# Kernel tuning notes

Measured on AMD Instinct MI355X. Metric: run time of the kernel, lower is better.

Reference implementation:

```python
import jax, jax.numpy as jnp
import numpy as np

NUM_EXPERTS = 8
TOP_K = 2
N_EMBD = 1024
BLOCKING = 128
D_FFN = ((4 * N_EMBD // TOP_K) + BLOCKING - 1) // BLOCKING * BLOCKING  # 2048


def setup_inputs() -> dict:
    key = jax.random.key(0)
    k_x, k_r, k_w1, k_w2 = jax.random.split(key, 4)
    B, S = 4, 2048
    x = jax.random.normal(k_x, (B, S, N_EMBD), dtype=jnp.float32)
    # nn.Linear weight layout: [out_features, in_features]
    router_w = jax.random.normal(k_r, (NUM_EXPERTS, N_EMBD), dtype=jnp.float32) * 0.02
    # trunc_normal(std=0.02, a=-0.06, b=0.06) approximated by clipped normal
    w1 = jnp.clip(jax.random.normal(k_w1, (N_EMBD, NUM_EXPERTS * D_FFN), dtype=jnp.float32) * 0.02, -0.06, 0.06)
    w2 = jnp.clip(jax.random.normal(k_w2, (NUM_EXPERTS * D_FFN, N_EMBD), dtype=jnp.float32) * 0.02, -0.06, 0.06)
    return {"x": x, "router_w": router_w, "w1": w1, "w2": w2}


def reference(x, router_w, w1, w2):
    B, S, D = x.shape
    T = B * S
    x_flat = x.reshape(T, D)

    # Router
    router_logits = x_flat @ router_w.T                       # [T, E]
    router_probs = jax.nn.softmax(router_logits.astype(jnp.float32), axis=-1)
    expert_weights, selected_experts = jax.lax.top_k(router_probs, TOP_K)  # [T, K]
    expert_weights = expert_weights / expert_weights.sum(axis=-1, keepdims=True)
    expert_weights = expert_weights.astype(x.dtype)

    # Combine weights c[t, e] = sum_k weight[t, k] * [sel[t, k] == e]
    combine = jnp.zeros((T, NUM_EXPERTS), dtype=x.dtype)
    combine = combine.at[jnp.arange(T)[:, None], selected_experts].add(expert_weights)

    # Expert FFNs (math equivalent of block-sparse sdd/gelu/dsd + scatter-combine)
    w1r = w1.reshape(D, NUM_EXPERTS, D_FFN)
    w2r = w2.reshape(NUM_EXPERTS, D_FFN, D)
    out_flat = jnp.zeros((T, D), dtype=x.dtype)
    for e in range(NUM_EXPERTS):
        h = jax.nn.gelu(x_flat @ w1r[:, e, :], approximate=False)  # [T, d_ffn]
        out_flat = out_flat + combine[:, e:e + 1] * (h @ w2r[e])
    output = out_flat.reshape(B, S, D)

    # Aux losses
    router_z_loss = jnp.mean(jax.nn.logsumexp(router_logits, axis=-1) ** 2)
    p_i = router_probs.mean(axis=0)                           # [E]
    f_i = jnp.zeros((NUM_EXPERTS,), dtype=x.dtype).at[selected_experts.reshape(-1)].add(
        jnp.float32(1.0) / (T * TOP_K))
    load_balance_loss = NUM_EXPERTS * jnp.dot(f_i, p_i.astype(x.dtype))

    return output, router_z_loss, load_balance_loss, f_i
```

## Files before the change

### kernel.cpp

```cpp
#include <hip/hip_runtime.h>
#include <hip/hip_bf16.h>
#include <math.h>

#define T_TOK   8192
#define D_MODEL 1024
#define DFFN    2048
#define N_EXP   8
#define NASSIGN (T_TOK*2)

#define TM 256
#define BN 256
#define BK 64
#define TILE_MAX 72

#define WS_ZSUM     0
#define WS_PSUM     4
#define WS_COUNTS   64
#define WS_CURSOR   96
#define WS_OFFS     128
#define WS_NTILES   160
#define WS_QHEAD    164
#define WS_QTOTAL   168
#define WS_DONE1    256
#define WS_TMAP     1024
#define WS_QITEMS   2560
#define WS_SEL      8192
#define WS_WGT      73728
#define WS_AIDX     139264
#define WS_AW       204800
#define WS_XB       270336
#define WS_W1T      (WS_XB + 16777216)
#define WS_W2T      (WS_W1T + 33554432)
#define WS_H        (WS_W2T + 33554432)

typedef __attribute__((ext_vector_type(8))) short bf16x8;
typedef __attribute__((ext_vector_type(4))) float f32x4;
typedef __attribute__((ext_vector_type(4))) unsigned int u32x4;

static __device__ __forceinline__ unsigned short f2bf(float f) {
    unsigned int u = __builtin_bit_cast(unsigned int, f);
    u += 0x7fffu + ((u >> 16) & 1u);
    return (unsigned short)(u >> 16);
}

static __device__ __forceinline__ void gll16(const unsigned short* g, unsigned short* l) {
    __builtin_amdgcn_global_load_lds(
        (const __attribute__((address_space(1))) unsigned int*)g,
        (__attribute__((address_space(3))) unsigned int*)l, 16, 0, 0);
}

static __device__ __forceinline__ int frag_off(int row, int kc) {
    return (row * 8 + (kc ^ (row & 7))) * 8;
}

__global__ __launch_bounds__(256) void transpose_cvt_kernel(
    const float* __restrict__ in, unsigned short* __restrict__ out, int K, int N)
{
    int e = blockIdx.z;
    const float* inp = in + (size_t)e * K * N;
    unsigned short* outp = out + (size_t)e * K * N;
    __shared__ unsigned short tile[64][68];
    int k0 = blockIdx.y * 64, n0 = blockIdx.x * 64;
    int tid = threadIdx.x;
    int r = tid >> 4, c4 = (tid & 15) * 4;
    #pragma unroll
    for (int p = 0; p < 4; ++p) {
        int k = r + p * 16;
        float4 v = *(const float4*)(inp + (size_t)(k0 + k) * N + n0 + c4);
        tile[k][c4+0] = f2bf(v.x);
        tile[k][c4+1] = f2bf(v.y);
        tile[k][c4+2] = f2bf(v.z);
        tile[k][c4+3] = f2bf(v.w);
    }
    __syncthreads();
    int n = tid >> 2, kc = (tid & 3) * 16;
    unsigned short t[16];
    #pragma unroll
    for (int j = 0; j < 16; ++j) t[j] = tile[kc + j][n];
    unsigned short* o = outp + (size_t)(n0 + n) * K + k0 + kc;
    *(u32x4*)o       = *(u32x4*)t;
    *(u32x4*)(o + 8) = *(u32x4*)(t + 8);
}

__global__ __launch_bounds__(256) void router_kernel(
    const float* __restrict__ x, const float* __restrict__ rw,
    float* zsum, float* psum, int* counts, int* sel, float* wgt,
    unsigned short* __restrict__ xb)
{
    __shared__ float xs[32*129];
    __shared__ float rs[8*129];
    __shared__ float lg[32*9];
    __shared__ float blk_p[8];
    __shared__ int   blk_c[8];
    __shared__ float blk_z;
    int tid = threadIdx.x;
    if (tid < 8) { blk_p[tid] = 0.f; blk_c[tid] = 0; }
    if (tid == 8) blk_z = 0.f;
    int tb = blockIdx.x * 32;
    int tt = tid >> 3, e = tid & 7;
    float acc = 0.f;
    for (int c = 0; c < 8; ++c) {
        int c0 = c * 128;
        #pragma unroll
        for (int p = 0; p < 16; ++p) {
            int flat = p * 256 + tid;
            int r = flat >> 7, col = flat & 127;
            xs[r*129 + col] = x[(size_t)(tb + r)*D_MODEL + c0 + col];
        }
        #pragma unroll
        for (int p = 0; p < 4; ++p) {
            int flat = p * 256 + tid;
            int er = flat >> 7, col = flat & 127;
            rs[er*129 + col] = rw[(size_t)er*D_MODEL + c0 + col];
        }
        __syncthreads();
        {
            int rr = tid >> 3, cc = (tid & 7) * 16;
            unsigned short tmp[16];
            #pragma unroll
            for (int j = 0; j < 16; ++j) tmp[j] = f2bf(xs[rr*129 + cc + j]);
            unsigned short* o = xb + (size_t)(tb + rr)*D_MODEL + c0 + cc;
            *(u32x4*)o       = *(u32x4*)tmp;
            *(u32x4*)(o + 8) = *(u32x4*)(tmp + 8);
        }
        #pragma unroll 8
        for (int i = 0; i < 128; ++i)
            acc += xs[tt*129 + i] * rs[e*129 + i];
        __syncthreads();
    }
    lg[tt*9 + e] = acc;
    __syncthreads();
    if (tid < 32) {
        int t = tb + tid;
        float l[8], p[8];
        float mx = -1e30f;
        #pragma unroll
        for (int j = 0; j < 8; ++j) { l[j] = lg[tid*9 + j]; mx = fmaxf(mx, l[j]); }
        float se = 0.f;
        #pragma unroll
        for (int j = 0; j < 8; ++j) { p[j] = expf(l[j] - mx); se += p[j]; }
        float inv = 1.f / se;
        #pragma unroll
        for (int j = 0; j < 8; ++j) p[j] *= inv;
        float lse = mx + logf(se);
        atomicAdd(&blk_z, lse*lse);
        #pragma unroll
        for (int j = 0; j < 8; ++j) atomicAdd(&blk_p[j], p[j]);
        int i0 = 0; float b0 = p[0];
        #pragma unroll
        for (int j = 1; j < 8; ++j) if (p[j] > b0) { b0 = p[j]; i0 = j; }
        int i1 = -1; float b1 = -1.f;
        #pragma unroll
        for (int j = 0; j < 8; ++j) if (j != i0 && p[j] > b1) { b1 = p[j]; i1 = j; }
        float s = b0 + b1;
        sel[t*2+0] = i0; sel[t*2+1] = i1;
        wgt[t*2+0] = b0 / s; wgt[t*2+1] = b1 / s;
        atomicAdd(&blk_c[i0], 1); atomicAdd(&blk_c[i1], 1);
    }
    __syncthreads();
    if (tid < 8) {
        atomicAdd(&counts[tid], blk_c[tid]);
        unsafeAtomicAdd(&psum[tid], blk_p[tid]);
    }
    if (tid == 8) unsafeAtomicAdd(zsum, blk_z);
}

__global__ void finalize_kernel(const int* counts, const float* psum, const float* zsum,
                                int* offs, int* ntiles, int* tmap, int* qitems,
                                int* qtotal, float* out_tail)
{
    if (threadIdx.x != 0) return;
    int off = 0, nt = 0;
    float lb = 0.f;
    for (int e = 0; e < N_EXP; ++e) {
        int c = counts[e];
        offs[e] = off;
        for (int m0 = 0; m0 < c; m0 += TM) {
            tmap[nt*4+0] = e;
            tmap[nt*4+1] = off + m0;
            tmap[nt*4+2] = min(TM, c - m0);
            tmap[nt*4+3] = 0;
            nt++;
        }
        float fi = (float)c / (float)NASSIGN;
        out_tail[2 + e] = fi;
        lb += fi * (psum[e] / (float)T_TOK);
        off += c;
    }
    *ntiles = nt;
    int q = 0;
    for (int t = 0; t < nt; ++t)
        for (int nb = 0; nb < DFFN/BN; ++nb)
            qitems[q++] = (0 << 14) | (t << 4) | nb;
    for (int t = 0; t < nt; ++t)
        for (int nb = 0; nb < D_MODEL/BN; ++nb)
            qitems[q++] = (1 << 14) | (t << 4) | nb;
    *qtotal = q;
    out_tail[0] = zsum[0] / (float)T_TOK;
    out_tail[1] = (float)N_EXP * lb;
}

__global__ __launch_bounds__(256) void scatter_kernel(
    const int* __restrict__ sel, const float* __restrict__ wgt,
    const int* __restrict__ offs, int* cursor, int* aidx, float* aw)
{
    int t = blockIdx.x * 256 + threadIdx.x;
    if (t >= T_TOK) return;
    #pragma unroll
    for (int k = 0; k < 2; ++k) {
        int e = sel[t*2 + k];
        int pos = atomicAdd(&cursor[e], 1);
        int r = offs[e] + pos;
        aidx[r] = t;
        aw[r] = wgt[t*2 + k];
    }
}


static __device__ __forceinline__ void gemm1_tile(
    int e, int gr, int valid, int n0,
    const unsigned short* __restrict__ xb, const unsigned short* __restrict__ w1t,
    const int* __restrict__ aidx, unsigned short* __restrict__ H,
    unsigned short (*As)[TM*BK], unsigned short (*Bs)[TM*BK], int tid)
{
    int lane = tid & 63, wave = tid >> 6;
    int wm = (wave >> 2) * 128, wn = (wave & 3) * 64;
    int q = lane >> 4, r16 = lane & 15;
    f32x4 acc[8][4];
    #pragma unroll
    for (int i = 0; i < 8; ++i)
        #pragma unroll
        for (int j = 0; j < 4; ++j) acc[i][j] = (f32x4){0.f, 0.f, 0.f, 0.f};

    const unsigned short* aga[4];
    const unsigned short* bga[4];
    int coff[4];
    #pragma unroll
    for (int u = 0; u < 4; ++u) {
        int cc = tid + u*512;
        int m = cc >> 3, kl = cc & 7;
        int kg = kl ^ (m & 7);
        int tok = aidx[gr + min(m, valid - 1)];
        aga[u] = xb + (size_t)tok * D_MODEL + kg*8;
        bga[u] = w1t + ((size_t)(e * DFFN + n0 + m)) * D_MODEL + kg*8;
        coff[u] = cc * 8;
    }

    const int NK = D_MODEL / BK;
    #pragma unroll
    for (int u = 0; u < 4; ++u) gll16(aga[u], &As[0][coff[u]]);
    #pragma unroll
    for (int u = 0; u < 4; ++u) gll16(bga[u], &Bs[0][coff[u]]);

    int cur = 0;
    for (int kt = 0; kt < NK; ++kt) {
        if (kt + 1 < NK) {
            int ko = (kt + 1) * BK;
            #pragma unroll
            for (int u = 0; u < 4; ++u) gll16(aga[u] + ko, &As[cur^1][coff[u]]);
            #pragma unroll
            for (int u = 0; u < 4; ++u) gll16(bga[u] + ko, &Bs[cur^1][coff[u]]);
            asm volatile("s_waitcnt vmcnt(8)" ::: "memory");
        } else {
            asm volatile("s_waitcnt vmcnt(0)" ::: "memory");
        }
        __builtin_amdgcn_sched_barrier(0);
        __builtin_amdgcn_s_barrier();
        asm volatile("" ::: "memory");
        const unsigned short* Ab = &As[cur][0];
        const unsigned short* Bb = &Bs[cur][0];
        __builtin_amdgcn_s_setprio(1);
        #pragma unroll
        for (int kh = 0; kh < 2; ++kh) {
            bf16x8 af[8], bfr[4];
            #pragma unroll
            for (int im = 0; im < 8; ++im)
                af[im] = *(const bf16x8*)&Ab[frag_off(wm + im*16 + r16, q + 4*kh)];
            #pragma unroll
            for (int in = 0; in < 4; ++in)
                bfr[in] = *(const bf16x8*)&Bb[frag_off(wn + in*16 + r16, q + 4*kh)];
            #pragma unroll
            for (int im = 0; im < 8; ++im)
                #pragma unroll
                for (int in = 0; in < 4; ++in)
                    acc[im][in] = __builtin_amdgcn_mfma_f32_16x16x32_bf16(af[im], bfr[in], acc[im][in], 0, 0, 0);
        }
        __builtin_amdgcn_s_setprio(0);
        asm volatile("" ::: "memory");
        __builtin_amdgcn_sched_barrier(0);
        __builtin_amdgcn_s_barrier();
        cur ^= 1;
    }
    #pragma unroll
    for (int im = 0; im < 8; ++im) {
        #pragma unroll
        for (int reg = 0; reg < 4; ++reg) {
            int m = wm + im*16 + q*4 + reg;
            if (m < valid) {
                size_t rowbase = (size_t)(gr + m) * DFFN + n0 + wn;
                #pragma unroll
                for (int in = 0; in < 4; ++in) {
                    float v = acc[im][in][reg];
                    float g = 0.5f * v * (1.0f + erff(v * 0.70710678118654752f));
                    H[rowbase + in*16 + r16] = f2bf(g);
                }
            }
        }
    }
}

static __device__ __forceinline__ void gemm2_tile(
    int e, int gr, int valid, int n0,
    const unsigned short* __restrict__ H, const unsigned short* __restrict__ w2t,
    const int* __restrict__ aidx, const float* __restrict__ aw,
    unsigned short (*As)[TM*BK], unsigned short (*Bs)[TM*BK],
    float* __restrict__ out, int tid)
{
    int lane = tid & 63, wave = tid >> 6;
    int wm = (wave >> 2) * 128, wn = (wave & 3) * 64;
    int q = lane >> 4, r16 = lane & 15;
    f32x4 acc[8][4];
    #pragma unroll
    for (int i = 0; i < 8; ++i)
        #pragma unroll
        for (int j = 0; j < 4; ++j) acc[i][j] = (f32x4){0.f, 0.f, 0.f, 0.f};

    const unsigned short* aga[4];
    const unsigned short* bga[4];
    int coff[4];
    #pragma unroll
    for (int u = 0; u < 4; ++u) {
        int cc = tid + u*512;
        int m = cc >> 3, kl = cc & 7;
        int kg = kl ^ (m & 7);
        aga[u] = H + (size_t)(gr + min(m, valid - 1)) * DFFN + kg*8;
        bga[u] = w2t + (size_t)e * (DFFN * D_MODEL) + (size_t)(n0 + m) * DFFN + kg*8;
        coff[u] = cc * 8;
    }

    const int NK = DFFN / BK;
    #pragma unroll
    for (int u = 0; u < 4; ++u) gll16(aga[u], &As[0][coff[u]]);
    #pragma unroll
    for (int u = 0; u < 4; ++u) gll16(bga[u], &Bs[0][coff[u]]);

    int cur = 0;
    for (int kt = 0; kt < NK; ++kt) {
        if (kt + 1 < NK) {
            int ko = (kt + 1) * BK;
            #pragma unroll
            for (int u = 0; u < 4; ++u) gll16(aga[u] + ko, &As[cur^1][coff[u]]);
            #pragma unroll
            for (int u = 0; u < 4; ++u) gll16(bga[u] + ko, &Bs[cur^1][coff[u]]);
            asm volatile("s_waitcnt vmcnt(8)" ::: "memory");
        } else {
            asm volatile("s_waitcnt vmcnt(0)" ::: "memory");
        }
        __builtin_amdgcn_sched_barrier(0);
        __builtin_amdgcn_s_barrier();
        asm volatile("" ::: "memory");
        const unsigned short* Ab = &As[cur][0];
        const unsigned short* Bb = &Bs[cur][0];
        __builtin_amdgcn_s_setprio(1);
        #pragma unroll
        for (int kh = 0; kh < 2; ++kh) {
            bf16x8 af[8], bfr[4];
            #pragma unroll
            for (int im = 0; im < 8; ++im)
                af[im] = *(const bf16x8*)&Ab[frag_off(wm + im*16 + r16, q + 4*kh)];
            #pragma unroll
            for (int in = 0; in < 4; ++in)
                bfr[in] = *(const bf16x8*)&Bb[frag_off(wn + in*16 + r16, q + 4*kh)];
            #pragma unroll
            for (int im = 0; im < 8; ++im)
                #pragma unroll
                for (int in = 0; in < 4; ++in)
                    acc[im][in] = __builtin_amdgcn_mfma_f32_16x16x32_bf16(af[im], bfr[in], acc[im][in], 0, 0, 0);
        }
        __builtin_amdgcn_s_setprio(0);
        asm volatile("" ::: "memory");
        __builtin_amdgcn_sched_barrier(0);
        __builtin_amdgcn_s_barrier();
        cur ^= 1;
    }
    #pragma unroll
    for (int im = 0; im < 8; ++im) {
        #pragma unroll
        for (int reg = 0; reg < 4; ++reg) {
            int m = wm + im*16 + q*4 + reg;
            if (m < valid) {
                int t = aidx[gr + m];
                float w = aw[gr + m];
                float* orow = out + (size_t)t*D_MODEL + n0 + wn;
                #pragma unroll
                for (int in = 0; in < 4; ++in)
                    unsafeAtomicAdd(&orow[in*16 + r16], w * acc[im][in][reg]);
            }
        }
    }
}

__global__ __launch_bounds__(512, 1) void moe_gemm_kernel(
    const unsigned short* __restrict__ xb, const unsigned short* __restrict__ w1t,
    const unsigned short* __restrict__ w2t, unsigned short* __restrict__ H,
    const int* __restrict__ aidx, const float* __restrict__ aw,
    const int* __restrict__ tmap, const int* __restrict__ qitems,
    int* qhead, const int* qtotal, int* done1, float* __restrict__ out)
{
    __shared__ unsigned short As[2][TM*BK];
    __shared__ unsigned short Bs[2][TM*BK];
    __shared__ int s_item;
    int tid = threadIdx.x;
    int qt = *qtotal;
    for (;;) {
        __syncthreads();
        if (tid == 0) s_item = atomicAdd(qhead, 1);
        __syncthreads();
        int it = s_item;
        if (it >= qt) return;
        int item = qitems[it];
        int type = item >> 14;
        int tile = (item >> 4) & 1023;
        int nb   = item & 15;
        int e     = tmap[tile*4+0];
        int gr    = tmap[tile*4+1];
        int valid = tmap[tile*4+2];
        if (type == 0) {
            gemm1_tile(e, gr, valid, nb * BN, xb, w1t, aidx, H, As, Bs, tid);
            __threadfence();
            __syncthreads();
            if (tid == 0) atomicAdd(&done1[tile], 1);
        } else {
            if (tid == 0) {
                while (__hip_atomic_load(done1 + tile, __ATOMIC_ACQUIRE,
                                         __HIP_MEMORY_SCOPE_AGENT) < DFFN/BN)
                    __builtin_amdgcn_s_sleep(8);
            }
            __syncthreads();
            __threadfence();
            gemm2_tile(e, gr, valid, nb * BN, H, w2t, aidx, aw, As, Bs, out, tid);
        }
    }
}

__global__ __launch_bounds__(512, 1) void gemm1_fb_kernel(
    const unsigned short* __restrict__ xb, const unsigned short* __restrict__ w1t,
    const int* __restrict__ aidx, const int* __restrict__ tmap,
    const int* __restrict__ ntiles, unsigned short* __restrict__ H)
{
    int bid = blockIdx.x;
    int xcd = bid & 7;
    int jj  = bid >> 3;
    int tile = (jj >> 3) * 8 + xcd;
    int n0   = (jj & 7) * BN;
    if (tile >= *ntiles) return;
    __shared__ unsigned short As[2][TM*BK];
    __shared__ unsigned short Bs[2][TM*BK];
    gemm1_tile(tmap[tile*4+0], tmap[tile*4+1], tmap[tile*4+2], n0,
               xb, w1t, aidx, H, As, Bs, threadIdx.x);
}

__global__ __launch_bounds__(512, 1) void gemm2_fb_kernel(
    const unsigned short* __restrict__ H, const unsigned short* __restrict__ w2t,
    const int* __restrict__ aidx, const float* __restrict__ aw,
    const int* __restrict__ tmap, const int* __restrict__ ntiles,
    float* __restrict__ out)
{
    int bid = blockIdx.x;
    int xcd = bid & 7;
    int jj  = bid >> 3;
    int tile = (jj >> 2) * 8 + xcd;
    int n0   = (jj & 3) * BN;
    if (tile >= *ntiles) return;
    __shared__ unsigned short As[2][TM*BK];
    __shared__ unsigned short Bs[2][TM*BK];
    gemm2_tile(tmap[tile*4+0], tmap[tile*4+1], tmap[tile*4+2], n0,
               H, w2t, aidx, aw, As, Bs, out, threadIdx.x);
}

extern "C" void kernel_launch(void* const* d_in, const int* in_sizes, int n_in,
                              void* d_out, int out_size, void* d_ws, size_t ws_size,
                              hipStream_t stream)
{
    const float* x  = (const float*)d_in[0];
    const float* rw = (const float*)d_in[1];
    const float* w1 = (const float*)d_in[2];
    const float* w2 = (const float*)d_in[3];
    float* out = (float*)d_out;
    char* ws = (char*)d_ws;
    float* zsum   = (float*)(ws + WS_ZSUM);
    float* psum   = (float*)(ws + WS_PSUM);
    int*   counts = (int*)(ws + WS_COUNTS);
    int*   cursor = (int*)(ws + WS_CURSOR);
    int*   offs   = (int*)(ws + WS_OFFS);
    int*   ntiles = (int*)(ws + WS_NTILES);
    int*   qhead  = (int*)(ws + WS_QHEAD);
    int*   qtotal = (int*)(ws + WS_QTOTAL);
    int*   done1  = (int*)(ws + WS_DONE1);
    int*   tmap   = (int*)(ws + WS_TMAP);
    int*   qitems = (int*)(ws + WS_QITEMS);
    int*   sel    = (int*)(ws + WS_SEL);
    float* wgt    = (float*)(ws + WS_WGT);
    int*   aidx   = (int*)(ws + WS_AIDX);
    float* aw     = (float*)(ws + WS_AW);
    unsigned short* xb  = (unsigned short*)(ws + WS_XB);
    unsigned short* w1t = (unsigned short*)(ws + WS_W1T);
    unsigned short* w2t = (unsigned short*)(ws + WS_W2T);
    unsigned short* H   = (unsigned short*)(ws + WS_H);

    hipMemsetAsync(d_out, 0, (size_t)T_TOK * D_MODEL * sizeof(float), stream);
    hipMemsetAsync(ws, 0, 2560, stream);

    transpose_cvt_kernel<<<dim3(16384/64, 1024/64, 1), 256, 0, stream>>>(w1, w1t, 1024, 16384);
    transpose_cvt_kernel<<<dim3(1024/64, 2048/64, 8), 256, 0, stream>>>(w2, w2t, 2048, 1024);

    router_kernel<<<T_TOK/32, 256, 0, stream>>>(x, rw, zsum, psum, counts, sel, wgt, xb);
    finalize_kernel<<<1, 64, 0, stream>>>(counts, psum, zsum, offs, ntiles, tmap,
                                          qitems, qtotal, out + (size_t)T_TOK * D_MODEL);
    scatter_kernel<<<T_TOK/256, 256, 0, stream>>>(sel, wgt, offs, cursor, aidx, aw);

    static int coopGrid = -2;
    if (coopGrid == -2) {
        int nb = 0;
        hipError_t oe = hipOccupancyMaxActiveBlocksPerMultiprocessor(
            &nb, moe_gemm_kernel, 512, 0);
        if (oe != hipSuccess || nb < 1) {
            coopGrid = -1;
        } else {
            hipDeviceProp_t prop;
            int cus = 256;
            if (hipGetDeviceProperties(&prop, 0) == hipSuccess)
                cus = prop.multiProcessorCount;
            int cap = nb * cus;
            coopGrid = cap < 256 ? cap : 256;
            if (coopGrid < 1) coopGrid = -1;
        }
    }

    bool launched = false;
    if (coopGrid > 0) {
        void* args[] = { (void*)&xb, (void*)&w1t, (void*)&w2t, (void*)&H,
                         (void*)&aidx, (void*)&aw, (void*)&tmap, (void*)&qitems,
                         (void*)&qhead, (void*)&qtotal, (void*)&done1, (void*)&out };
        hipError_t le = hipLaunchCooperativeKernel(
            (const void*)moe_gemm_kernel, dim3(coopGrid), dim3(512), args, 0, stream);
        if (le == hipSuccess) launched = true;
        else coopGrid = -1;
    }
    if (!launched) {
        gemm1_fb_kernel<<<dim3(TILE_MAX * (DFFN/BN)), 512, 0, stream>>>(
            xb, w1t, aidx, tmap, ntiles, H);
        gemm2_fb_kernel<<<dim3(TILE_MAX * (D_MODEL/BN)), 512, 0, stream>>>(
            H, w2t, aidx, aw, tmap, ntiles, out);
    }
}
```

Before: 611.1 us.

## Split gemm2 work items along K into halves and relax fence ordering

Each gemm2 tile item is split into two K-halves (split-K), doubling the number of gemm2 work items in the persistent queue so the tail of the schedule is better balanced across CUs. The epilogue presumably accumulates into the output atomically, so both halves can add their partial sums. The change also replaces full thread fences with a release fence on the producer side and a relaxed spin load on the consumer side, which reduces synchronization overhead. The risk is extra atomic traffic on the output and weaker memory-ordering guarantees when reading H.

```diff
diff --git a/kernel.cpp b/kernel.cpp
--- a/kernel.cpp
+++ b/kernel.cpp
@@ -193,8 +193,8 @@
         for (int nb = 0; nb < DFFN/BN; ++nb)
             qitems[q++] = (0 << 14) | (t << 4) | nb;
     for (int t = 0; t < nt; ++t)
-        for (int nb = 0; nb < D_MODEL/BN; ++nb)
-            qitems[q++] = (1 << 14) | (t << 4) | nb;
+        for (int sub = 0; sub < 8; ++sub)
+            qitems[q++] = (1 << 14) | (t << 4) | sub;
     *qtotal = q;
     out_tail[0] = zsum[0] / (float)T_TOK;
     out_tail[1] = (float)N_EXP * lb;
@@ -310,7 +310,7 @@
 }
 
 static __device__ __forceinline__ void gemm2_tile(
-    int e, int gr, int valid, int n0,
+    int e, int gr, int valid, int n0, int k0,
     const unsigned short* __restrict__ H, const unsigned short* __restrict__ w2t,
     const int* __restrict__ aidx, const float* __restrict__ aw,
     unsigned short (*As)[TM*BK], unsigned short (*Bs)[TM*BK],
@@ -333,12 +333,12 @@
         int cc = tid + u*512;
         int m = cc >> 3, kl = cc & 7;
         int kg = kl ^ (m & 7);
-        aga[u] = H + (size_t)(gr + min(m, valid - 1)) * DFFN + kg*8;
-        bga[u] = w2t + (size_t)e * (DFFN * D_MODEL) + (size_t)(n0 + m) * DFFN + kg*8;
+        aga[u] = H + (size_t)(gr + min(m, valid - 1)) * DFFN + k0 + kg*8;
+        bga[u] = w2t + (size_t)e * (DFFN * D_MODEL) + (size_t)(n0 + m) * DFFN + k0 + kg*8;
         coff[u] = cc * 8;
     }
 
-    const int NK = DFFN / BK;
+    const int NK = 1024 / BK;
     #pragma unroll
     for (int u = 0; u < 4; ++u) gll16(aga[u], &As[0][coff[u]]);
     #pragma unroll
@@ -421,24 +421,26 @@
         int item = qitems[it];
         int type = item >> 14;
         int tile = (item >> 4) & 1023;
-        int nb   = item & 15;
+        int sub  = item & 15;
         int e     = tmap[tile*4+0];
         int gr    = tmap[tile*4+1];
         int valid = tmap[tile*4+2];
         if (type == 0) {
-            gemm1_tile(e, gr, valid, nb * BN, xb, w1t, aidx, H, As, Bs, tid);
-            __threadfence();
+            gemm1_tile(e, gr, valid, sub * BN, xb, w1t, aidx, H, As, Bs, tid);
+            __builtin_amdgcn_fence(__ATOMIC_RELEASE, "agent");
             __syncthreads();
             if (tid == 0) atomicAdd(&done1[tile], 1);
         } else {
             if (tid == 0) {
-                while (__hip_atomic_load(done1 + tile, __ATOMIC_ACQUIRE,
+                while (__hip_atomic_load(done1 + tile, __ATOMIC_RELAXED,
                                          __HIP_MEMORY_SCOPE_AGENT) < DFFN/BN)
                     __builtin_amdgcn_s_sleep(8);
             }
             __syncthreads();
-            __threadfence();
-            gemm2_tile(e, gr, valid, nb * BN, H, w2t, aidx, aw, As, Bs, out, tid);
+            asm volatile("" ::: "memory");
+            int nb = sub & 3, kh = sub >> 2;
+            gemm2_tile(e, gr, valid, nb * BN, kh * 1024,
+                       H, w2t, aidx, aw, As, Bs, out, tid);
         }
     }
 }
@@ -474,7 +476,10 @@
     if (tile >= *ntiles) return;
     __shared__ unsigned short As[2][TM*BK];
     __shared__ unsigned short Bs[2][TM*BK];
-    gemm2_tile(tmap[tile*4+0], tmap[tile*4+1], tmap[tile*4+2], n0,
+    gemm2_tile(tmap[tile*4+0], tmap[tile*4+1], tmap[tile*4+2], n0, 0,
+               H, w2t, aidx, aw, As, Bs, out, threadIdx.x);
+    __syncthreads();
+    gemm2_tile(tmap[tile*4+0], tmap[tile*4+1], tmap[tile*4+2], n0, 1024,
                H, w2t, aidx, aw, As, Bs, out, threadIdx.x);
 }
 
```

Result: slower. 657.8 us (+7.6%).
